# Kernel optimization log

Measured on AMD Instinct MI355X. Metric: run time of the kernel, lower is better.

The kernel has to match this reference:

```python
import jax, jax.numpy as jnp
import numpy as np

B, S, D, H = 2, 2048, 1024, 16
HD = D // H                 # head_dim = 64
BLOCK = 16                  # _DEFAULT_BLOCK_SIZE
NB = S // BLOCK             # max_blocks_per_seq = 128
WINDOW = 512
NEG = jnp.float32(-1e30)


def setup_inputs() -> dict:
    key = jax.random.key(0)
    ks = jax.random.split(key, 5)
    x = jax.random.normal(ks[0], (B, S, D), jnp.float32)
    scale = D ** -0.5
    wq = jax.random.normal(ks[1], (D, D), jnp.float32) * scale
    wk = jax.random.normal(ks[2], (D, D), jnp.float32) * scale
    wv = jax.random.normal(ks[3], (D, D), jnp.float32) * scale
    wo = jax.random.normal(ks[4], (D, D), jnp.float32) * scale
    # sequential paged layout (matches the module's synthesized-cache fallback)
    block_tables = jnp.arange(B * NB, dtype=jnp.int32).reshape(B, NB)
    slot_mapping = jnp.arange(B * S, dtype=jnp.int32)
    context_lens = jnp.full((B,), S, dtype=jnp.int32)
    return {"x": x, "wq": wq, "wk": wk, "wv": wv, "wo": wo,
            "block_tables": block_tables, "slot_mapping": slot_mapping,
            "context_lens": context_lens, "window_size": WINDOW}


def reference(x, wq, wk, wv, wo, block_tables, slot_mapping, context_lens, window_size):
    b, s, d = x.shape
    # Q/K/V projections (nn.Linear, bias=False: y = x @ W^T)
    q = (x @ wq.T).reshape(b, s, H, HD)
    k = (x @ wk.T).reshape(b, s, H, HD)
    v = (x @ wv.T).reshape(b, s, H, HD)

    # ---- memopt_C.write_cache: scatter K/V into the physical slot pool ----
    num_slots = b * s
    key_cache = jnp.zeros((num_slots, H, HD), x.dtype).at[slot_mapping].set(k.reshape(-1, H, HD))
    value_cache = jnp.zeros((num_slots, H, HD), x.dtype).at[slot_mapping].set(v.reshape(-1, H, HD))

    # ---- dynamic_sparse_attention: read KV through block_tables ----
    t = jnp.arange(s)
    # physical slot of logical token t of sequence b: block_tables[b, t//BLOCK]*BLOCK + t%BLOCK
    slots = block_tables[:, t // BLOCK].astype(jnp.int32) * BLOCK + (t % BLOCK)[None, :].astype(jnp.int32)  # [B,S]
    kc = key_cache[slots]    # [B,S,H,HD]
    vc = value_cache[slots]  # [B,S,H,HD]

    scores = jnp.einsum('bqhd,bkhd->bhqk', q, kc) * (HD ** -0.5)  # [B,H,S,S]
    qpos = t[:, None]
    kpos = t[None, :]
    # causal + window-limited visibility (window_size tokens of history)
    vis = (kpos <= qpos) & (qpos - kpos < window_size)            # [S,S]
    ctx = t[None, :] < context_lens[:, None]                       # [B,S]
    mask = vis[None, None, :, :] & ctx[:, None, None, :]
    scores = jnp.where(mask, scores, NEG)
    attn = jax.nn.softmax(scores, axis=-1)
    out = jnp.einsum('bhqk,bkhd->bqhd', attn, vc).reshape(b, s, d)
    return out @ wo.T
```

## Files before the change

kernel.cpp:

```cpp
#include <hip/hip_runtime.h>

typedef __attribute__((ext_vector_type(4))) float  f32x4;
typedef __attribute__((ext_vector_type(8))) short  bf16x8;

typedef __attribute__((address_space(3))) void lds_void_t;
typedef __attribute__((address_space(1))) void g_void_t;

#define S_LEN  2048
#define DMODEL 1024
#define NHEAD  16
#define HDIM   64
#define NBLK   128
#define BATCH  2
#define KT     64
#define VP     72

__device__ __forceinline__ short f2bf(float f) {
  union { float f; unsigned u; } v; v.f = f;
  unsigned r = v.u + 0x7fffu + ((v.u >> 16) & 1u);
  return (short)(r >> 16);
}

__global__ __launch_bounds__(256) void cvt_all_kernel(
    const float* __restrict__ x,  const float* __restrict__ wq,
    const float* __restrict__ wk, const float* __restrict__ wv,
    const float* __restrict__ wo,
    short* __restrict__ xb,  short* __restrict__ wqb,
    short* __restrict__ wkb, short* __restrict__ wvb,
    short* __restrict__ wob) {
  const long i = ((long)blockIdx.x * 256 + threadIdx.x) * 8;
  const float* s; short* d; long off;
  if (i < 4194304L)      { s = x;  d = xb;  off = i; }
  else if (i < 5242880L) { s = wq; d = wqb; off = i - 4194304L; }
  else if (i < 6291456L) { s = wk; d = wkb; off = i - 5242880L; }
  else if (i < 7340032L) { s = wv; d = wvb; off = i - 6291456L; }
  else                   { s = wo; d = wob; off = i - 7340032L; }
  f32x4 a = *(const f32x4*)(s + off);
  f32x4 b = *(const f32x4*)(s + off + 4);
  bf16x8 o;
  o[0]=f2bf(a[0]); o[1]=f2bf(a[1]); o[2]=f2bf(a[2]); o[3]=f2bf(a[3]);
  o[4]=f2bf(b[0]); o[5]=f2bf(b[1]); o[6]=f2bf(b[2]); o[7]=f2bf(b[3]);
  *(bf16x8*)(d + off) = o;
}

__global__ __launch_bounds__(512, 2) void gemm8_kernel(
    const short* __restrict__ A,
    const short* __restrict__ W0, const short* __restrict__ W1, const short* __restrict__ W2,
    const int* __restrict__ slot_map,
    short* __restrict__ qbuf, short* __restrict__ kcache, short* __restrict__ vcache)
{
  extern __shared__ short smem[];

  const int m0 = blockIdx.x * 256;
  const int n0 = blockIdx.y * 192;
  const short* Ag = A + (size_t)m0 * DMODEL;

  const int tid  = threadIdx.x;
  const int wave = tid >> 6, lane = tid & 63;
  const int l15 = lane & 15, lg = lane >> 4;
  const int wr = wave >> 2, wc = wave & 3;
  const int swz = l15 & 7;

  short* const A0s = smem;
  short* const B0s = smem + 16384;
  short* const A1s = smem + 28672;
  short* const B1s = smem + 45056;

  f32x4 acc[8][3];
#pragma unroll
  for (int m = 0; m < 8; m++)
#pragma unroll
    for (int n = 0; n < 3; n++) acc[m][n] = (f32x4)0.f;

#define STAGE_A(DST, K0, P) {                                                              \
    const int gidx = (P) * 512 + tid;                                                      \
    const int r = gidx >> 3;                                                               \
    const int cs = (gidx & 7) ^ (r & 7);                                                   \
    __builtin_amdgcn_global_load_lds((g_void_t*)(Ag + (size_t)r * DMODEL + (K0) + cs * 8), \
        (lds_void_t*)((DST) + ((P) * 512 + wave * 64) * 8), 16, 0, 0); }

#define STAGE_B(DST, K0, P) {                                                              \
    const int gidx = (P) * 512 + tid;                                                      \
    const int r = gidx >> 3;                                                               \
    const int grow = n0 + r;                                                               \
    const short* wb = (grow < 1024) ? W0 : (grow < 2048) ? W1 : W2;                        \
    const int cs = (gidx & 7) ^ (r & 7);                                                   \
    __builtin_amdgcn_global_load_lds((g_void_t*)(wb + (size_t)(grow & 1023) * DMODEL + (K0) + cs * 8), \
        (lds_void_t*)((DST) + ((P) * 512 + wave * 64) * 8), 16, 0, 0); }

#define PHASE_BAR() do {                                        \
    asm volatile("" ::: "memory");                              \
    __builtin_amdgcn_s_barrier();                               \
    asm volatile("" ::: "memory");                              \
  } while (0)

  STAGE_B(B0s, 0, 0); STAGE_B(B0s, 0, 1); STAGE_B(B0s, 0, 2);
  STAGE_A(A0s, 0, 0); STAGE_A(A0s, 0, 2); STAGE_A(A0s, 0, 1); STAGE_A(A0s, 0, 3);
  asm volatile("s_waitcnt vmcnt(0)" ::: "memory");
  __builtin_amdgcn_s_barrier();
  asm volatile("" ::: "memory");

  const int NT = DMODEL / 64;
  for (int t = 0; t < NT; ++t) {
    const bool stg = (t + 1 < NT);
    short* const Ac = (t & 1) ? A1s : A0s;
    short* const Bc = (t & 1) ? B1s : B0s;
    short* const An = (t & 1) ? A0s : A1s;
    short* const Bn = (t & 1) ? B0s : B1s;
    const int kn = (t + 1) * 64;

    bf16x8 af[4][2], bfr[3][2];

#pragma unroll
    for (int nt = 0; nt < 3; ++nt) {
      const int row = wc * 48 + nt * 16 + l15;
#pragma unroll
      for (int ks = 0; ks < 2; ++ks)
        bfr[nt][ks] = *(const bf16x8*)(Bc + row * 64 + (((ks * 4 + lg) ^ swz) << 3));
    }
#pragma unroll
    for (int mi = 0; mi < 4; ++mi) {
      const int row = wr * 128 + mi * 16 + l15;
#pragma unroll
      for (int ks = 0; ks < 2; ++ks)
        af[mi][ks] = *(const bf16x8*)(Ac + row * 64 + (((ks * 4 + lg) ^ swz) << 3));
    }
    if (stg) { STAGE_B(Bn, kn, 0); STAGE_B(Bn, kn, 1); STAGE_B(Bn, kn, 2);
               STAGE_A(An, kn, 0); STAGE_A(An, kn, 2); }
    PHASE_BAR();
    __builtin_amdgcn_s_setprio(1);
#pragma unroll
    for (int mi = 0; mi < 4; ++mi)
#pragma unroll
      for (int nt = 0; nt < 3; ++nt)
#pragma unroll
        for (int ks = 0; ks < 2; ++ks)
          acc[mi][nt] = __builtin_amdgcn_mfma_f32_16x16x32_bf16(
              af[mi][ks], bfr[nt][ks], acc[mi][nt], 0, 0, 0);
    __builtin_amdgcn_s_setprio(0);
    if (stg) { asm volatile("s_waitcnt vmcnt(5)" ::: "memory"); }
    else     { asm volatile("s_waitcnt vmcnt(0)" ::: "memory"); }
    PHASE_BAR();

#pragma unroll
    for (int mi = 0; mi < 4; ++mi) {
      const int row = wr * 128 + 64 + mi * 16 + l15;
#pragma unroll
      for (int ks = 0; ks < 2; ++ks)
        af[mi][ks] = *(const bf16x8*)(Ac + row * 64 + (((ks * 4 + lg) ^ swz) << 3));
    }
    if (stg) { STAGE_A(An, kn, 1); STAGE_A(An, kn, 3); }
    PHASE_BAR();
    __builtin_amdgcn_s_setprio(1);
#pragma unroll
    for (int mi = 0; mi < 4; ++mi)
#pragma unroll
      for (int nt = 0; nt < 3; ++nt)
#pragma unroll
        for (int ks = 0; ks < 2; ++ks)
          acc[4 + mi][nt] = __builtin_amdgcn_mfma_f32_16x16x32_bf16(
              af[mi][ks], bfr[nt][ks], acc[4 + mi][nt], 0, 0, 0);
    __builtin_amdgcn_s_setprio(0);
    if (stg) { asm volatile("s_waitcnt vmcnt(2)" ::: "memory"); }
    else     { asm volatile("s_waitcnt vmcnt(0)" ::: "memory"); }
    PHASE_BAR();
  }
#undef STAGE_A
#undef STAGE_B
#undef PHASE_BAR

#pragma unroll
  for (int mf = 0; mf < 8; ++mf) {
    const int rowb = m0 + wr * 128 + mf * 16 + lg * 4;
#pragma unroll
    for (int r4 = 0; r4 < 4; ++r4) {
      const int row = rowb + r4;
      const int slot = slot_map[row];
#pragma unroll
      for (int nt = 0; nt < 3; ++nt) {
        const int col = n0 + wc * 48 + nt * 16 + l15;
        const short bv = f2bf(acc[mf][nt][r4]);
        if (col < DMODEL)
          qbuf[(size_t)row * DMODEL + col] = bv;
        else if (col < 2 * DMODEL)
          kcache[(size_t)slot * DMODEL + (col - DMODEL)] = bv;
        else
          vcache[(size_t)slot * DMODEL + (col - 2 * DMODEL)] = bv;
      }
    }
  }
}

__global__ __launch_bounds__(256, 2) void gemm1_kernel(
    const short* __restrict__ A, const short* __restrict__ W,
    float* __restrict__ outf)
{
  extern __shared__ short smem1[];

  const int m0 = blockIdx.x * 128;
  const int n0 = blockIdx.y * 128;
  const short* Ag = A + (size_t)m0 * DMODEL;
  const short* Bg = W + (size_t)n0 * DMODEL;

  const int tid = threadIdx.x;
  const int wave = tid >> 6, lane = tid & 63;
  const int l15 = lane & 15, lg = lane >> 4;
  const int wr = wave >> 1, wc = wave & 1;
  const int swz = l15 & 7;

  short* const As0 = smem1;
  short* const Bs0 = smem1 + 8192;
  short* const As1 = smem1 + 16384;
  short* const Bs1 = smem1 + 24576;

  f32x4 acc[4][4];
#pragma unroll
  for (int m = 0; m < 4; m++)
#pragma unroll
    for (int n = 0; n < 4; n++) acc[m][n] = (f32x4)0.f;

#define STG1(LA, LB, K0) {                                                                 \
    _Pragma("unroll") for (int p = 0; p < 4; ++p) {                                        \
      const int u = p * 256 + tid; const int r = u >> 3; const int cs = (u & 7) ^ (r & 7); \
      __builtin_amdgcn_global_load_lds((g_void_t*)(Ag + (size_t)r * DMODEL + (K0) + cs * 8), \
          (lds_void_t*)((LA) + (p * 256 + wave * 64) * 8), 16, 0, 0); }                    \
    _Pragma("unroll") for (int p = 0; p < 4; ++p) {                                        \
      const int u = p * 256 + tid; const int r = u >> 3; const int cs = (u & 7) ^ (r & 7); \
      __builtin_amdgcn_global_load_lds((g_void_t*)(Bg + (size_t)r * DMODEL + (K0) + cs * 8), \
          (lds_void_t*)((LB) + (p * 256 + wave * 64) * 8), 16, 0, 0); } }

  STG1(As0, Bs0, 0);
  asm volatile("s_waitcnt vmcnt(0)" ::: "memory");
  __builtin_amdgcn_s_barrier();
  asm volatile("" ::: "memory");

  for (int t = 0; t < 16; ++t) {
    const int cur = t & 1;
    short* const Ac = cur ? As1 : As0;
    short* const Bc = cur ? Bs1 : Bs0;
    short* const An = cur ? As0 : As1;
    short* const Bn = cur ? Bs0 : Bs1;
    if (t + 1 < 16) {
      STG1(An, Bn, (t + 1) * 64);
      asm volatile("s_waitcnt vmcnt(8)" ::: "memory");
    } else {
      asm volatile("s_waitcnt vmcnt(0)" ::: "memory");
    }
    asm volatile("" ::: "memory");
    __builtin_amdgcn_s_barrier();
    asm volatile("" ::: "memory");

    bf16x8 af[4][2], bfr[4][2];
#pragma unroll
    for (int m4 = 0; m4 < 4; ++m4) {
      const int row = wr * 64 + m4 * 16 + l15;
#pragma unroll
      for (int ks = 0; ks < 2; ++ks)
        af[m4][ks] = *(const bf16x8*)(Ac + row * 64 + (((ks * 4 + lg) ^ swz) << 3));
    }
#pragma unroll
    for (int n4 = 0; n4 < 4; ++n4) {
      const int row = wc * 64 + n4 * 16 + l15;
#pragma unroll
      for (int ks = 0; ks < 2; ++ks)
        bfr[n4][ks] = *(const bf16x8*)(Bc + row * 64 + (((ks * 4 + lg) ^ swz) << 3));
    }
    __builtin_amdgcn_s_setprio(1);
#pragma unroll
    for (int m4 = 0; m4 < 4; ++m4)
#pragma unroll
      for (int n4 = 0; n4 < 4; ++n4)
#pragma unroll
        for (int ks = 0; ks < 2; ++ks)
          acc[m4][n4] = __builtin_amdgcn_mfma_f32_16x16x32_bf16(af[m4][ks], bfr[n4][ks], acc[m4][n4], 0, 0, 0);
    __builtin_amdgcn_s_setprio(0);

    asm volatile("" ::: "memory");
    __builtin_amdgcn_s_barrier();
    asm volatile("" ::: "memory");
  }
#undef STG1

#pragma unroll
  for (int m4 = 0; m4 < 4; ++m4) {
    const int rowb = m0 + wr * 64 + m4 * 16 + lg * 4;
#pragma unroll
    for (int n4 = 0; n4 < 4; ++n4) {
      const int col = n0 + wc * 64 + n4 * 16 + l15;
#pragma unroll
      for (int r4 = 0; r4 < 4; ++r4)
        outf[(size_t)(rowb + r4) * DMODEL + col] = acc[m4][n4][r4];
    }
  }
}

__global__ __launch_bounds__(512, 4) void attn_kernel(
    const short* __restrict__ qbuf,
    const short* __restrict__ kcache, const short* __restrict__ vcache,
    const int* __restrict__ block_tables, const int* __restrict__ context_lens,
    const int* __restrict__ window_size,
    short* __restrict__ attn_out)
{
  __shared__ short Ks[2][KT * 64];
  __shared__ short Vt[2][HDIM * VP];
  __shared__ short Pb[8 * 16 * VP];

  const int b = blockIdx.z, h = blockIdx.y;
  const int bx = (b & 1) ? ((int)gridDim.x - 1 - (int)blockIdx.x) : (int)blockIdx.x;
  const int q0 = bx * 128;
  const int ctx = context_lens[b];
  const int ws  = window_size[0];
  const int* bt = block_tables + b * NBLK;

  const int tid  = threadIdx.x;
  const int wave = tid >> 6, lane = tid & 63;
  const int l15 = lane & 15, lg = lane >> 4;
  const int qw = q0 + wave * 16;

  const short* qp = qbuf + ((size_t)(b * S_LEN + qw + l15)) * DMODEL + h * HDIM;
  const bf16x8 qf0 = *(const bf16x8*)(qp + lg * 8);
  const bf16x8 qf1 = *(const bf16x8*)(qp + 32 + lg * 8);

  f32x4 oacc[4];
  float lrow[4];
#pragma unroll
  for (int i = 0; i < 4; i++) { oacc[i] = (f32x4)0.f; lrow[i] = 0.f; }

  int kstart = q0 - ws + 1; if (kstart < 0) kstart = 0; kstart &= ~(KT - 1);
  int kend = q0 + 128; if (kend > ctx) kend = ctx;

  const int kr = tid >> 3;
  const int dc = (tid & 7) << 3;
  const float rscale = 0.125f;
  const float FM = 12.f;
  short* pw = Pb + wave * (16 * VP);
  const int swz = (l15 & 7) << 4;

  bf16x8 kreg = (bf16x8)0, vreg = (bf16x8)0;
  {
    const int key = kstart + kr;
    if (key < ctx) {
      const int slot = bt[key >> 4] * 16 + (key & 15);
      kreg = *(const bf16x8*)(kcache + (size_t)slot * DMODEL + h * HDIM + dc);
      vreg = *(const bf16x8*)(vcache + (size_t)slot * DMODEL + h * HDIM + dc);
    }
  }

  int tix = 0;
  for (int kt = kstart; kt < kend; kt += KT, ++tix) {
    short* const KsB = Ks[tix & 1];
    short* const VtB = Vt[tix & 1];
    *(bf16x8*)((char*)KsB + kr * 128 + ((dc * 2) ^ ((kr & 7) << 4))) = kreg;
    const int vcol = (kr + dc) & 63;
#pragma unroll
    for (int j = 0; j < 8; j++) VtB[(dc + j) * VP + vcol] = vreg[j];
    kreg = (bf16x8)0; vreg = (bf16x8)0;
    if (kt + KT < kend) {
      const int key = kt + KT + kr;
      if (key < ctx) {
        const int slot = bt[key >> 4] * 16 + (key & 15);
        kreg = *(const bf16x8*)(kcache + (size_t)slot * DMODEL + h * HDIM + dc);
        vreg = *(const bf16x8*)(vcache + (size_t)slot * DMODEL + h * HDIM + dc);
      }
    }
    __syncthreads();

    if ((kt > qw + 15) || (kt + (KT - 1) <= qw - ws)) continue;

    f32x4 sacc[4];
#pragma unroll
    for (int cg = 0; cg < 4; cg++) sacc[cg] = (f32x4)0.f;
#pragma unroll
    for (int cg = 0; cg < 4; cg++) {
      const char* kp = (const char*)KsB + (cg * 16 + l15) * 128;
      const bf16x8 k0 = *(const bf16x8*)(kp + ((lg * 16) ^ swz));
      const bf16x8 k1 = *(const bf16x8*)(kp + ((64 + lg * 16) ^ swz));
      sacc[cg] = __builtin_amdgcn_mfma_f32_16x16x32_bf16(qf0, k0, sacc[cg], 0, 0, 0);
      sacc[cg] = __builtin_amdgcn_mfma_f32_16x16x32_bf16(qf1, k1, sacc[cg], 0, 0, 0);
    }

    const bool fullvis = (kt + (KT - 1) <= qw) && (qw + 15 - kt < ws) && (kt + (KT - 1) < ctx);

    if (fullvis) {
#pragma unroll
      for (int r = 0; r < 4; r++) {
        const float e0 = __expf(sacc[0][r] * rscale - FM);
        const float e1 = __expf(sacc[1][r] * rscale - FM);
        const float e2 = __expf(sacc[2][r] * rscale - FM);
        const float e3 = __expf(sacc[3][r] * rscale - FM);
        lrow[r] += (e0 + e1) + (e2 + e3);
        short* pr = pw + (lg * 4 + r) * VP + l15;
        pr[0]  = f2bf(e0); pr[16] = f2bf(e1);
        pr[32] = f2bf(e2); pr[48] = f2bf(e3);
      }
    } else {
#pragma unroll
      for (int r = 0; r < 4; r++) {
        const int qrow = qw + lg * 4 + r;
        const int key0 = kt + l15;
        const bool ok0 = (key0      <= qrow) && (qrow - key0      < ws) && (key0      < ctx);
        const bool ok1 = (key0 + 16 <= qrow) && (qrow - key0 - 16 < ws) && (key0 + 16 < ctx);
        const bool ok2 = (key0 + 32 <= qrow) && (qrow - key0 - 32 < ws) && (key0 + 32 < ctx);
        const bool ok3 = (key0 + 48 <= qrow) && (qrow - key0 - 48 < ws) && (key0 + 48 < ctx);
        const float e0 = ok0 ? __expf(sacc[0][r] * rscale - FM) : 0.f;
        const float e1 = ok1 ? __expf(sacc[1][r] * rscale - FM) : 0.f;
        const float e2 = ok2 ? __expf(sacc[2][r] * rscale - FM) : 0.f;
        const float e3 = ok3 ? __expf(sacc[3][r] * rscale - FM) : 0.f;
        lrow[r] += (e0 + e1) + (e2 + e3);
        short* pr = pw + (lg * 4 + r) * VP + l15;
        pr[0]  = f2bf(e0); pr[16] = f2bf(e1);
        pr[32] = f2bf(e2); pr[48] = f2bf(e3);
      }
    }

    asm volatile("s_waitcnt lgkmcnt(0)" ::: "memory");

#pragma unroll
    for (int kk = 0; kk < 2; kk++) {
      const bf16x8 pa = *(const bf16x8*)(pw + l15 * VP + kk * 32 + lg * 8);
#pragma unroll
      for (int dn = 0; dn < 4; dn++) {
        const int vrow = dn * 16 + l15;
        const int roff = (kk * 32 + lg * 8 + (vrow & ~7)) & 63;
        const bf16x8 vb = *(const bf16x8*)(VtB + vrow * VP + roff);
        oacc[dn] = __builtin_amdgcn_mfma_f32_16x16x32_bf16(pa, vb, oacc[dn], 0, 0, 0);
      }
    }
  }

#pragma unroll
  for (int r = 0; r < 4; r++) {
    float ls = lrow[r];
    ls += __shfl_xor(ls, 1); ls += __shfl_xor(ls, 2);
    ls += __shfl_xor(ls, 4); ls += __shfl_xor(ls, 8);
    const float inv = 1.f / fmaxf(ls, 1e-30f);
    const int row = qw + lg * 4 + r;
    short* op = attn_out + ((size_t)(b * S_LEN + row)) * DMODEL + h * HDIM;
#pragma unroll
    for (int dn = 0; dn < 4; dn++)
      op[dn * 16 + l15] = f2bf(oacc[dn][r] * inv);
  }
}

extern "C" void kernel_launch(void* const* d_in, const int* in_sizes, int n_in,
                              void* d_out, int out_size, void* d_ws, size_t ws_size,
                              hipStream_t stream) {
  const float* x  = (const float*)d_in[0];
  const float* wq = (const float*)d_in[1];
  const float* wk = (const float*)d_in[2];
  const float* wv = (const float*)d_in[3];
  const float* wo = (const float*)d_in[4];
  const int* block_tables = (const int*)d_in[5];
  const int* slot_mapping = (const int*)d_in[6];
  const int* context_lens = (const int*)d_in[7];
  const int* window_size  = (const int*)d_in[8];
  float* out = (float*)d_out;

  char* ws = (char*)d_ws;
  short* xb     = (short*)(ws + (size_t)( 0 << 20));
  short* wqb    = (short*)(ws + (size_t)( 8 << 20));
  short* wkb    = (short*)(ws + (size_t)(10 << 20));
  short* wvb    = (short*)(ws + (size_t)(12 << 20));
  short* wob    = (short*)(ws + (size_t)(14 << 20));
  short* qbuf   = (short*)(ws + (size_t)(16 << 20));
  short* kcache = (short*)(ws + (size_t)(24 << 20));
  short* vcache = (short*)(ws + (size_t)(32 << 20));
  short* abuf   = (short*)(ws + (size_t)(40 << 20));

  static bool ginit = [] {
    hipFuncSetAttribute(reinterpret_cast<const void*>(&gemm8_kernel),
                        hipFuncAttributeMaxDynamicSharedMemorySize, 114688);
    hipFuncSetAttribute(reinterpret_cast<const void*>(&gemm1_kernel),
                        hipFuncAttributeMaxDynamicSharedMemorySize, 65536);
    return true;
  }();
  (void)ginit;

  cvt_all_kernel<<<4096, 256, 0, stream>>>(x, wq, wk, wv, wo, xb, wqb, wkb, wvb, wob);

  gemm8_kernel<<<dim3(16, 16), 512, 114688, stream>>>(xb, wqb, wkb, wvb, slot_mapping,
                                                      qbuf, kcache, vcache);

  attn_kernel<<<dim3(S_LEN / 128, NHEAD, BATCH), 512, 0, stream>>>(
      qbuf, kcache, vcache, block_tables, context_lens, window_size, abuf);

  gemm1_kernel<<<dim3(32, 8), 256, 65536, stream>>>(abuf, wob, out);
}
```

Before: 90.90 us.

## Shrink QKV GEMM tile to 128 rows and single-buffer attention K/V tiles

The QKV projection GEMM moves from 256x192 tiles with 512 threads to 128x192 tiles with 256 threads. This doubles the grid to 512 blocks for better CU coverage and cuts LDS per block. The staging schedule and vmcnt waits are rebalanced to match. The attention kernel drops double-buffered K/V LDS tiles for single buffers guarded by a __syncthreads each iteration, which lowers LDS use but adds a barrier and less overlap between staging and compute.

```diff
diff --git a/kernel.cpp b/kernel.cpp
--- a/kernel.cpp
+++ b/kernel.cpp
@@ -43,7 +43,7 @@
   *(bf16x8*)(d + off) = o;
 }
 
-__global__ __launch_bounds__(512, 2) void gemm8_kernel(
+__global__ __launch_bounds__(256, 2) void gemm8_kernel(
     const short* __restrict__ A,
     const short* __restrict__ W0, const short* __restrict__ W1, const short* __restrict__ W2,
     const int* __restrict__ slot_map,
@@ -51,20 +51,20 @@
 {
   extern __shared__ short smem[];
 
-  const int m0 = blockIdx.x * 256;
+  const int m0 = blockIdx.x * 128;
   const int n0 = blockIdx.y * 192;
   const short* Ag = A + (size_t)m0 * DMODEL;
 
   const int tid  = threadIdx.x;
   const int wave = tid >> 6, lane = tid & 63;
   const int l15 = lane & 15, lg = lane >> 4;
-  const int wr = wave >> 2, wc = wave & 3;
+  const int wc = wave;
   const int swz = l15 & 7;
 
   short* const A0s = smem;
-  short* const B0s = smem + 16384;
-  short* const A1s = smem + 28672;
-  short* const B1s = smem + 45056;
+  short* const B0s = smem + 8192;
+  short* const A1s = smem + 20480;
+  short* const B1s = smem + 28672;
 
   f32x4 acc[8][3];
 #pragma unroll
@@ -73,20 +73,20 @@
     for (int n = 0; n < 3; n++) acc[m][n] = (f32x4)0.f;
 
 #define STAGE_A(DST, K0, P) {                                                              \
-    const int gidx = (P) * 512 + tid;                                                      \
+    const int gidx = (P) * 256 + tid;                                                      \
     const int r = gidx >> 3;                                                               \
     const int cs = (gidx & 7) ^ (r & 7);                                                   \
     __builtin_amdgcn_global_load_lds((g_void_t*)(Ag + (size_t)r * DMODEL + (K0) + cs * 8), \
-        (lds_void_t*)((DST) + ((P) * 512 + wave * 64) * 8), 16, 0, 0); }
+        (lds_void_t*)((DST) + ((P) * 256 + wave * 64) * 8), 16, 0, 0); }
 
 #define STAGE_B(DST, K0, P) {                                                              \
-    const int gidx = (P) * 512 + tid;                                                      \
+    const int gidx = (P) * 256 + tid;                                                      \
     const int r = gidx >> 3;                                                               \
     const int grow = n0 + r;                                                               \
     const short* wb = (grow < 1024) ? W0 : (grow < 2048) ? W1 : W2;                        \
     const int cs = (gidx & 7) ^ (r & 7);                                                   \
     __builtin_amdgcn_global_load_lds((g_void_t*)(wb + (size_t)(grow & 1023) * DMODEL + (K0) + cs * 8), \
-        (lds_void_t*)((DST) + ((P) * 512 + wave * 64) * 8), 16, 0, 0); }
+        (lds_void_t*)((DST) + ((P) * 256 + wave * 64) * 8), 16, 0, 0); }
 
 #define PHASE_BAR() do {                                        \
     asm volatile("" ::: "memory");                              \
@@ -95,7 +95,8 @@
   } while (0)
 
   STAGE_B(B0s, 0, 0); STAGE_B(B0s, 0, 1); STAGE_B(B0s, 0, 2);
-  STAGE_A(A0s, 0, 0); STAGE_A(A0s, 0, 2); STAGE_A(A0s, 0, 1); STAGE_A(A0s, 0, 3);
+  STAGE_B(B0s, 0, 3); STAGE_B(B0s, 0, 4); STAGE_B(B0s, 0, 5);
+  STAGE_A(A0s, 0, 0); STAGE_A(A0s, 0, 1); STAGE_A(A0s, 0, 2); STAGE_A(A0s, 0, 3);
   asm volatile("s_waitcnt vmcnt(0)" ::: "memory");
   __builtin_amdgcn_s_barrier();
   asm volatile("" ::: "memory");
@@ -120,13 +121,16 @@
     }
 #pragma unroll
     for (int mi = 0; mi < 4; ++mi) {
-      const int row = wr * 128 + mi * 16 + l15;
+      const int row = mi * 16 + l15;
 #pragma unroll
       for (int ks = 0; ks < 2; ++ks)
         af[mi][ks] = *(const bf16x8*)(Ac + row * 64 + (((ks * 4 + lg) ^ swz) << 3));
     }
-    if (stg) { STAGE_B(Bn, kn, 0); STAGE_B(Bn, kn, 1); STAGE_B(Bn, kn, 2);
-               STAGE_A(An, kn, 0); STAGE_A(An, kn, 2); }
+    if (stg) {
+      STAGE_B(Bn, kn, 0); STAGE_B(Bn, kn, 1); STAGE_B(Bn, kn, 2);
+      STAGE_B(Bn, kn, 3); STAGE_B(Bn, kn, 4); STAGE_B(Bn, kn, 5);
+      STAGE_A(An, kn, 0); STAGE_A(An, kn, 1);
+    }
     PHASE_BAR();
     __builtin_amdgcn_s_setprio(1);
 #pragma unroll
@@ -138,18 +142,18 @@
           acc[mi][nt] = __builtin_amdgcn_mfma_f32_16x16x32_bf16(
               af[mi][ks], bfr[nt][ks], acc[mi][nt], 0, 0, 0);
     __builtin_amdgcn_s_setprio(0);
-    if (stg) { asm volatile("s_waitcnt vmcnt(5)" ::: "memory"); }
+    if (stg) { asm volatile("s_waitcnt vmcnt(8)" ::: "memory"); }
     else     { asm volatile("s_waitcnt vmcnt(0)" ::: "memory"); }
     PHASE_BAR();
 
 #pragma unroll
     for (int mi = 0; mi < 4; ++mi) {
-      const int row = wr * 128 + 64 + mi * 16 + l15;
+      const int row = 64 + mi * 16 + l15;
 #pragma unroll
       for (int ks = 0; ks < 2; ++ks)
         af[mi][ks] = *(const bf16x8*)(Ac + row * 64 + (((ks * 4 + lg) ^ swz) << 3));
     }
-    if (stg) { STAGE_A(An, kn, 1); STAGE_A(An, kn, 3); }
+    if (stg) { STAGE_A(An, kn, 2); STAGE_A(An, kn, 3); }
     PHASE_BAR();
     __builtin_amdgcn_s_setprio(1);
 #pragma unroll
@@ -171,7 +175,7 @@
 
 #pragma unroll
   for (int mf = 0; mf < 8; ++mf) {
-    const int rowb = m0 + wr * 128 + mf * 16 + lg * 4;
+    const int rowb = m0 + mf * 16 + lg * 4;
 #pragma unroll
     for (int r4 = 0; r4 < 4; ++r4) {
       const int row = rowb + r4;
@@ -301,8 +305,8 @@
     const int* __restrict__ window_size,
     short* __restrict__ attn_out)
 {
-  __shared__ short Ks[2][KT * 64];
-  __shared__ short Vt[2][HDIM * VP];
+  __shared__ short Ks[KT * 64];
+  __shared__ short Vt[HDIM * VP];
   __shared__ short Pb[8 * 16 * VP];
 
   const int b = blockIdx.z, h = blockIdx.y;
@@ -346,14 +350,12 @@
     }
   }
 
-  int tix = 0;
-  for (int kt = kstart; kt < kend; kt += KT, ++tix) {
-    short* const KsB = Ks[tix & 1];
-    short* const VtB = Vt[tix & 1];
-    *(bf16x8*)((char*)KsB + kr * 128 + ((dc * 2) ^ ((kr & 7) << 4))) = kreg;
+  for (int kt = kstart; kt < kend; kt += KT) {
+    __syncthreads();
+    *(bf16x8*)((char*)Ks + kr * 128 + ((dc * 2) ^ ((kr & 7) << 4))) = kreg;
     const int vcol = (kr + dc) & 63;
 #pragma unroll
-    for (int j = 0; j < 8; j++) VtB[(dc + j) * VP + vcol] = vreg[j];
+    for (int j = 0; j < 8; j++) Vt[(dc + j) * VP + vcol] = vreg[j];
     kreg = (bf16x8)0; vreg = (bf16x8)0;
     if (kt + KT < kend) {
       const int key = kt + KT + kr;
@@ -372,7 +374,7 @@
     for (int cg = 0; cg < 4; cg++) sacc[cg] = (f32x4)0.f;
 #pragma unroll
     for (int cg = 0; cg < 4; cg++) {
-      const char* kp = (const char*)KsB + (cg * 16 + l15) * 128;
+      const char* kp = (const char*)Ks + (cg * 16 + l15) * 128;
       const bf16x8 k0 = *(const bf16x8*)(kp + ((lg * 16) ^ swz));
       const bf16x8 k1 = *(const bf16x8*)(kp + ((64 + lg * 16) ^ swz));
       sacc[cg] = __builtin_amdgcn_mfma_f32_16x16x32_bf16(qf0, k0, sacc[cg], 0, 0, 0);
@@ -422,7 +424,7 @@
       for (int dn = 0; dn < 4; dn++) {
         const int vrow = dn * 16 + l15;
         const int roff = (kk * 32 + lg * 8 + (vrow & ~7)) & 63;
-        const bf16x8 vb = *(const bf16x8*)(VtB + vrow * VP + roff);
+        const bf16x8 vb = *(const bf16x8*)(Vt + vrow * VP + roff);
         oacc[dn] = __builtin_amdgcn_mfma_f32_16x16x32_bf16(pa, vb, oacc[dn], 0, 0, 0);
       }
     }
@@ -469,7 +471,7 @@
 
   static bool ginit = [] {
     hipFuncSetAttribute(reinterpret_cast<const void*>(&gemm8_kernel),
-                        hipFuncAttributeMaxDynamicSharedMemorySize, 114688);
+                        hipFuncAttributeMaxDynamicSharedMemorySize, 81920);
     hipFuncSetAttribute(reinterpret_cast<const void*>(&gemm1_kernel),
                         hipFuncAttributeMaxDynamicSharedMemorySize, 65536);
     return true;
@@ -478,8 +480,8 @@
 
   cvt_all_kernel<<<4096, 256, 0, stream>>>(x, wq, wk, wv, wo, xb, wqb, wkb, wvb, wob);
 
-  gemm8_kernel<<<dim3(16, 16), 512, 114688, stream>>>(xb, wqb, wkb, wvb, slot_mapping,
-                                                      qbuf, kcache, vcache);
+  gemm8_kernel<<<dim3(32, 16), 256, 81920, stream>>>(xb, wqb, wkb, wvb, slot_mapping,
+                                                     qbuf, kcache, vcache);
 
   attn_kernel<<<dim3(S_LEN / 128, NHEAD, BATCH), 512, 0, stream>>>(
       qbuf, kcache, vcache, block_tables, context_lens, window_size, abuf);
```

New measurement: 90.56 us. About the same (-0.4%).
